# Kernel tuning notes

Measured on AMD Instinct MI355X. Metric: run time of the kernel, lower is better.

The kernel has to match this reference:

```python
import jax, jax.numpy as jnp
import numpy as np

N, IN_F, OUT_F = 8192, 512, 256
ALPHA = 0.2  # LeakyReLU negative slope
NEG_INF = -9e15


def setup_inputs() -> dict:
    key = jax.random.key(0)
    k1, k2, k3, k4 = jax.random.split(key, 4)
    input = jax.random.normal(k1, (N, IN_F), dtype=jnp.float32)
    adj = jax.random.randint(k2, (N, N), 0, 2, dtype=jnp.int32)
    # Xavier-like scale for params
    W = jax.random.normal(k3, (IN_F, OUT_F), dtype=jnp.float32) * (1.414 * np.sqrt(2.0 / (IN_F + OUT_F)))
    a = jax.random.normal(k4, (2 * OUT_F, 1), dtype=jnp.float32) * (1.414 * np.sqrt(2.0 / (2 * OUT_F + 1)))
    return {"input": input, "adj": adj, "W": W, "a": a}


def reference(input, adj, W, a):
    h = input @ W                                   # [N, F]
    a1, a2 = a[:OUT_F, 0], a[OUT_F:, 0]             # [F], [F]
    # e[i, j] = leakyrelu(h_i . a1 + h_j . a2) -- equivalent to concat+linear
    s1 = h @ a1                                     # [N]
    s2 = h @ a2                                     # [N]
    e = jax.nn.leaky_relu(s1[:, None] + s2[None, :], negative_slope=ALPHA)  # [N, N]
    e = jnp.where(adj > 0, e, NEG_INF)
    attention = jax.nn.softmax(e, axis=1)           # row-wise softmax
    # dropout p=0.0 / eval mode -> identity
    h_prime = attention @ h                          # [N, F]
    return jax.nn.elu(h_prime)                       # concat=True -> elu
```

## Files before the change

kernel.cpp:

```cpp
#include <hip/hip_runtime.h>
#include <stdint.h>

#define N_NODES 8192
#define IN_FEAT 512
#define OUT_FEAT 256
#define LOG2E 1.4426950408889634f

typedef __bf16 b16x8 __attribute__((ext_vector_type(8)));
typedef unsigned short u16x8v __attribute__((ext_vector_type(8)));
typedef float f32x4 __attribute__((ext_vector_type(4)));
typedef float f32x16 __attribute__((ext_vector_type(16)));

static __device__ __forceinline__ unsigned short f2bf(float f) {
    union { float f; uint32_t u; } v; v.f = f;
    uint32_t r = v.u + 0x7FFFu + ((v.u >> 16) & 1u);
    return (unsigned short)(r >> 16);
}

__global__ __launch_bounds__(256) void k_pack(const int* __restrict__ adj,
                                              unsigned char* __restrict__ bitsR) {
    size_t t = (size_t)blockIdx.x * 256 + threadIdx.x;
    const int4* a4 = (const int4*)adj + t * 2;
    int4 x0 = a4[0];
    int4 x1 = a4[1];
    unsigned b = (unsigned)(x0.x != 0)
               | ((unsigned)(x0.y != 0) << 1)
               | ((unsigned)(x0.z != 0) << 2)
               | ((unsigned)(x0.w != 0) << 3)
               | ((unsigned)(x1.x != 0) << 4)
               | ((unsigned)(x1.y != 0) << 5)
               | ((unsigned)(x1.z != 0) << 6)
               | ((unsigned)(x1.w != 0) << 7);
    bitsR[t] = (unsigned char)b;
}

__global__ __launch_bounds__(256) void k0_transpose_w(const float* __restrict__ W,
                                                      unsigned short* __restrict__ Wt) {
    int tid = blockIdx.x * 256 + threadIdx.x;
    int c = tid & (OUT_FEAT - 1);
    int k = tid >> 8;
    Wt[(size_t)c * IN_FEAT + k] = f2bf(W[(size_t)k * OUT_FEAT + c]);
}

__global__ __launch_bounds__(256) void k1_hgemm(const float* __restrict__ input,
                                                const unsigned short* __restrict__ Wt,
                                                const float* __restrict__ a_vec,
                                                unsigned short* __restrict__ hTf32,
                                                float* __restrict__ s1_raw,
                                                float* __restrict__ s2_raw) {
    int tid = threadIdx.x;
    int lane = tid & 63;
    int c = lane & 15, g = lane >> 4;
    int r0 = blockIdx.x * 64 + (tid >> 6) * 16;
    f32x4 acc[16];
#pragma unroll
    for (int t = 0; t < 16; ++t) acc[t] = (f32x4){0.f, 0.f, 0.f, 0.f};
    const float* arow = input + (size_t)(r0 + c) * IN_FEAT;
#pragma unroll 1
    for (int kk = 0; kk < IN_FEAT / 32; ++kk) {
        int kb = kk * 32 + 8 * g;
        float4 x0 = *(const float4*)(arow + kb);
        float4 x1 = *(const float4*)(arow + kb + 4);
        u16x8v au;
        au[0] = f2bf(x0.x); au[1] = f2bf(x0.y); au[2] = f2bf(x0.z); au[3] = f2bf(x0.w);
        au[4] = f2bf(x1.x); au[5] = f2bf(x1.y); au[6] = f2bf(x1.z); au[7] = f2bf(x1.w);
        b16x8 af = __builtin_bit_cast(b16x8, au);
#pragma unroll
        for (int t = 0; t < 16; ++t) {
            b16x8 bf = __builtin_bit_cast(b16x8,
                *(const u16x8v*)(Wt + (size_t)(16 * t + c) * IN_FEAT + kb));
            acc[t] = __builtin_amdgcn_mfma_f32_16x16x32_bf16(af, bf, acc[t], 0, 0, 0);
        }
    }
    float a1v[16], a2v[16];
#pragma unroll
    for (int t = 0; t < 16; ++t) {
        a1v[t] = a_vec[16 * t + c];
        a2v[t] = a_vec[OUT_FEAT + 16 * t + c];
    }
#pragma unroll
    for (int r = 0; r < 4; ++r) {
        float s1p = 0.f, s2p = 0.f;
#pragma unroll
        for (int t = 0; t < 16; ++t) { s1p += acc[t][r] * a1v[t]; s2p += acc[t][r] * a2v[t]; }
#pragma unroll
        for (int m = 1; m <= 8; m <<= 1) { s1p += __shfl_xor(s1p, m); s2p += __shfl_xor(s2p, m); }
        if (c == 0) {
            int row = r0 + 4 * g + r;
            s1_raw[row] = s1p;
            s2_raw[row] = s2p;
        }
    }
    int chunk16 = r0 >> 4;
    int lane_base = c + 32 * (g >> 1);
    int e0 = 4 * (g & 1);
#pragma unroll
    for (int t = 0; t < 16; ++t) {
        ushort4 pk;
        pk.x = f2bf(acc[t][0]); pk.y = f2bf(acc[t][1]);
        pk.z = f2bf(acc[t][2]); pk.w = f2bf(acc[t][3]);
        int lane_t = 16 * (t & 1) + lane_base;
        *(ushort4*)(hTf32 + ((size_t)(chunk16 * 8 + (t >> 1)) * 64 + lane_t) * 8 + e0) = pk;
    }
}

__global__ __launch_bounds__(256) void k2_prep(const float* __restrict__ s1_raw,
                                               const float* __restrict__ s2_raw,
                                               float* __restrict__ e12,
                                               float2* __restrict__ row2) {
    __shared__ float red[256];
    int tid = threadIdx.x;
    float m = -3.0e38f;
    for (int j = tid; j < N_NODES; j += 256) m = fmaxf(m, s2_raw[j]);
    red[tid] = m;
    __syncthreads();
    for (int s = 128; s > 0; s >>= 1) {
        if (tid < s) red[tid] = fmaxf(red[tid], red[tid + s]);
        __syncthreads();
    }
    float M2 = red[0];
    int i = blockIdx.x * 256 + tid;
    float s1 = s1_raw[i];
    float u = s1 + M2;
    float mi = fmaxf(u, 0.2f * u);
    row2[i] = make_float2(__builtin_amdgcn_exp2f((s1 - mi) * LOG2E),
                          __builtin_amdgcn_exp2f((0.2f * s1 - mi) * LOG2E));
    float s2 = s2_raw[i];
    e12[2 * i]     = __builtin_amdgcn_exp2f(s2 * LOG2E);
    e12[2 * i + 1] = __builtin_amdgcn_exp2f(0.2f * s2 * LOG2E);
}

__global__ __launch_bounds__(256, 4) void k3_flash(const uint32_t* __restrict__ maskR,
                                                   const unsigned short* __restrict__ hTf32,
                                                   const float* __restrict__ e12g,
                                                   const float2* __restrict__ row2,
                                                   float* __restrict__ pout,
                                                   float* __restrict__ rowpart) {
    __shared__ __align__(16) float le12[4096];

    int tid = threadIdx.x;
    int cq = tid >> 6, lane = tid & 63;
    int lr = lane & 31, lo = lane >> 5;
    int jq = blockIdx.x & 3;
    int rg = blockIdx.x >> 2;
    int rowbase = rg * 32;

#pragma unroll
    for (int q = 0; q < 4; ++q) {
        *(float4*)&le12[tid * 16 + q * 4] =
            *(const float4*)(e12g + (size_t)jq * 4096 + tid * 16 + q * 4);
    }
    float2 rc = row2[rowbase + lr];
    float E1r = rc.x, E2r = rc.y;
    __syncthreads();

    const int4* m4 = (const int4*)(maskR + (size_t)(rowbase + lr) * 256 + jq * 64);

    f32x16 acc0 = {0}, acc1 = {0};
    float lacc = 0.f;

#pragma unroll 1
    for (int kc8 = 0; kc8 < 16; ++kc8) {
        int4 mq = m4[kc8];
        uint32_t md[4] = {(uint32_t)mq.x, (uint32_t)mq.y, (uint32_t)mq.z, (uint32_t)mq.w};
#pragma unroll
        for (int sub = 0; sub < 8; ++sub) {
            int kc = kc8 * 8 + sub;
            int gchunk = jq * 128 + kc;
            const unsigned short* tb =
                hTf32 + ((size_t)(gchunk * 8 + 2 * cq) * 64 + lane) * 8;

            b16x8 bf0 = __builtin_bit_cast(b16x8, *(const u16x8v*)(tb));
            b16x8 bf1 = __builtin_bit_cast(b16x8, *(const u16x8v*)(tb + 512));

            float ev[16];
#pragma unroll
            for (int q = 0; q < 4; ++q)
                *(f32x4*)&ev[q * 4] = *(const f32x4*)&le12[(kc * 16 + 8 * lo) * 2 + q * 4];

            uint32_t mb = (md[sub >> 1] >> (16 * (sub & 1) + 8 * lo)) & 0xFFu;
            b16x8 af;
#pragma unroll
            for (int e = 0; e < 8; ++e) {
                float q0 = fmaxf(E1r * ev[2 * e], E2r * ev[2 * e + 1]);
                float p = (mb & (1u << e)) ? q0 : 0.f;
                lacc += p;
                af[e] = (__bf16)p;
            }

            acc0 = __builtin_amdgcn_mfma_f32_32x32x16_bf16(af, bf0, acc0, 0, 0, 0);
            acc1 = __builtin_amdgcn_mfma_f32_32x32x16_bf16(af, bf1, acc1, 0, 0, 0);
        }
    }

    float ltot = lacc + __shfl_xor(lacc, 32);
    if (cq == 0 && lo == 0) rowpart[jq * N_NODES + rowbase + lr] = ltot;

#pragma unroll
    for (int reg = 0; reg < 16; ++reg) {
        int row = (reg & 3) + 8 * (reg >> 2) + 4 * lo;
        size_t base = ((size_t)jq * N_NODES + rowbase + row) * OUT_FEAT + cq * 64 + lr;
        pout[base] = acc0[reg];
        pout[base + 32] = acc1[reg];
    }
}

__global__ __launch_bounds__(256) void k4_reduce(const float* __restrict__ pout,
                                                 const float* __restrict__ rowpart,
                                                 float* __restrict__ out) {
    int t = blockIdx.x * 256 + threadIdx.x;
    int row = t >> 8;
    float s = 0.f, l = 0.f;
#pragma unroll
    for (int q = 0; q < 4; ++q) {
        s += pout[(size_t)q * N_NODES * OUT_FEAT + t];
        l += rowpart[q * N_NODES + row];
    }
    float inv = (l > 0.f) ? 1.0f / l : 0.f;
    float x = s * inv;
    out[t] = (x > 0.f) ? x : (__builtin_amdgcn_exp2f(x * LOG2E) - 1.0f);
}

extern "C" void kernel_launch(void* const* d_in, const int* in_sizes, int n_in,
                              void* d_out, int out_size, void* d_ws, size_t ws_size,
                              hipStream_t stream) {
    const float* input = (const float*)d_in[0];
    const int* adj = (const int*)d_in[1];
    const float* W = (const float*)d_in[2];
    const float* a_vec = (const float*)d_in[3];
    float* out = (float*)d_out;

    char* ws = (char*)d_ws;
    unsigned short* Wt    = (unsigned short*)(ws);
    unsigned short* hTf32 = (unsigned short*)(ws + 262144);
    float*  e12     = (float*)(ws + 4456448);
    float2* row2    = (float2*)(ws + 4521984);
    float*  s1_raw  = (float*)(ws + 4587520);
    float*  s2_raw  = (float*)(ws + 4620288);
    unsigned char* bitsR = (unsigned char*)(ws + 4653056);
    float*  rowpart = (float*)(ws + 13041664);
    float*  pout    = (float*)(ws + 13172736);

    hipLaunchKernelGGL(k_pack, dim3(32768), dim3(256), 0, stream, adj, bitsR);
    hipLaunchKernelGGL(k0_transpose_w, dim3(512), dim3(256), 0, stream, W, Wt);
    hipLaunchKernelGGL(k1_hgemm, dim3(N_NODES / 64), dim3(256), 0, stream,
                       input, Wt, a_vec, hTf32, s1_raw, s2_raw);
    hipLaunchKernelGGL(k2_prep, dim3(32), dim3(256), 0, stream, s1_raw, s2_raw, e12, row2);
    hipLaunchKernelGGL(k3_flash, dim3(1024), dim3(256), 0, stream,
                       (const uint32_t*)bitsR, hTf32, e12, row2, pout, rowpart);
    hipLaunchKernelGGL(k4_reduce, dim3(N_NODES * OUT_FEAT / 256), dim3(256), 0, stream,
                       pout, rowpart, out);
}
```

Baseline: 177.3 us.

## Share attention-weight tile computation across waves via LDS instead of recomputing per wave

Before, each of the four waves built the full masked exp-weight A fragment for every k-chunk, so all four did the same work. Now each wave computes one of four chunks, writes it to shared memory, and after a barrier all waves read the four fragments and issue their MFMAs. Row sums are combined across waves through shared memory. This cuts VALU exp/mask work by four at the cost of two block barriers per group, extra LDS traffic, and less room for overlap between VALU and MFMA.

Result: faster. 161.0 us (-9.2%).

```diff
diff --git a/kernel.cpp b/kernel.cpp
--- a/kernel.cpp
+++ b/kernel.cpp
@@ -137,6 +137,8 @@
                                                    float* __restrict__ pout,
                                                    float* __restrict__ rowpart) {
     __shared__ __align__(16) float le12[4096];
+    __shared__ __align__(16) unsigned short laf[4][1024];
+    __shared__ float lsum[4][64];
 
     int tid = threadIdx.x;
     int cq = tid >> 6, lane = tid & 63;
@@ -164,21 +166,16 @@
         int4 mq = m4[kc8];
         uint32_t md[4] = {(uint32_t)mq.x, (uint32_t)mq.y, (uint32_t)mq.z, (uint32_t)mq.w};
 #pragma unroll
-        for (int sub = 0; sub < 8; ++sub) {
-            int kc = kc8 * 8 + sub;
-            int gchunk = jq * 128 + kc;
-            const unsigned short* tb =
-                hTf32 + ((size_t)(gchunk * 8 + 2 * cq) * 64 + lane) * 8;
-
-            b16x8 bf0 = __builtin_bit_cast(b16x8, *(const u16x8v*)(tb));
-            b16x8 bf1 = __builtin_bit_cast(b16x8, *(const u16x8v*)(tb + 512));
+        for (int h = 0; h < 2; ++h) {
+            int grp = kc8 * 2 + h;
+            int sl = h * 4 + cq;
+            int kc = kc8 * 8 + sl;
 
             float ev[16];
 #pragma unroll
             for (int q = 0; q < 4; ++q)
                 *(f32x4*)&ev[q * 4] = *(const f32x4*)&le12[(kc * 16 + 8 * lo) * 2 + q * 4];
-
-            uint32_t mb = (md[sub >> 1] >> (16 * (sub & 1) + 8 * lo)) & 0xFFu;
+            uint32_t mb = (md[sl >> 1] >> (16 * (sl & 1) + 8 * lo)) & 0xFFu;
             b16x8 af;
 #pragma unroll
             for (int e = 0; e < 8; ++e) {
@@ -187,14 +184,31 @@
                 lacc += p;
                 af[e] = (__bf16)p;
             }
-
-            acc0 = __builtin_amdgcn_mfma_f32_32x32x16_bf16(af, bf0, acc0, 0, 0, 0);
-            acc1 = __builtin_amdgcn_mfma_f32_32x32x16_bf16(af, bf1, acc1, 0, 0, 0);
+            *(u16x8v*)&laf[cq][lane * 8] = __builtin_bit_cast(u16x8v, af);
+            __syncthreads();
+
+            int gchunk0 = jq * 128 + grp * 4;
+#pragma unroll
+            for (int s = 0; s < 4; ++s) {
+                const unsigned short* tb =
+                    hTf32 + ((size_t)((gchunk0 + s) * 8 + 2 * cq) * 64 + lane) * 8;
+                b16x8 bf0 = __builtin_bit_cast(b16x8, *(const u16x8v*)(tb));
+                b16x8 bf1 = __builtin_bit_cast(b16x8, *(const u16x8v*)(tb + 512));
+                b16x8 afs = __builtin_bit_cast(b16x8, *(const u16x8v*)&laf[s][lane * 8]);
+                acc0 = __builtin_amdgcn_mfma_f32_32x32x16_bf16(afs, bf0, acc0, 0, 0, 0);
+                acc1 = __builtin_amdgcn_mfma_f32_32x32x16_bf16(afs, bf1, acc1, 0, 0, 0);
+            }
+            __syncthreads();
         }
     }
 
-    float ltot = lacc + __shfl_xor(lacc, 32);
-    if (cq == 0 && lo == 0) rowpart[jq * N_NODES + rowbase + lr] = ltot;
+    lsum[cq][lane] = lacc;
+    __syncthreads();
+    if (cq == 0) {
+        float l = lsum[0][lane] + lsum[1][lane] + lsum[2][lane] + lsum[3][lane];
+        float ltot = l + __shfl_xor(l, 32);
+        if (lo == 0) rowpart[jq * N_NODES + rowbase + lr] = ltot;
+    }
 
 #pragma unroll
     for (int reg = 0; reg < 16; ++reg) {
```
